# Performance work log

Hardware: AMD Instinct MI355X
Metric: run time of the kernel (lower is better)

Reference implementation:

```python
import jax, jax.numpy as jnp
import numpy as np

B, N, D, H, L, R = 2, 2048, 1024, 16, 3, 2
HID = int(D * 2.67)
NASH_ITERS, SINK_ITERS = 3, 10
EPS = 1e-6


def _rmsnorm(x, w):
    return x * w * jax.lax.rsqrt(jnp.mean(x * x, axis=-1, keepdims=True) + EPS)


def _sinkhorn(logits):
    # Sinkhorn-Knopp projection of exp(logits) to a doubly-stochastic matrix
    M = jnp.exp(logits)
    for _ in range(SINK_ITERS):
        M = M / jnp.sum(M, axis=1, keepdims=True)
        M = M / jnp.sum(M, axis=0, keepdims=True)
    return M


def _swiglu(x, wg, wu, wd):
    return (jax.nn.silu(x @ wg) * (x @ wu)) @ wd


def _attention(xl, wq, wk, Wv):
    # causal multi-head attention at one scale; V projection (Wv) is shared across scales
    b, n, d = xl.shape
    dh = d // H
    q = (xl @ wq).reshape(b, n, H, dh)
    k = (xl @ wk).reshape(b, n, H, dh)
    v = (xl @ Wv).reshape(b, n, H, dh)
    scores = jnp.einsum('bqhd,bkhd->bhqk', q, k) / jnp.asarray(float(np.sqrt(dh)), xl.dtype)
    mask = jnp.tril(jnp.ones((n, n), bool))
    scores = jnp.where(mask, scores, jnp.asarray(-1e9, xl.dtype))
    p = jax.nn.softmax(scores, axis=-1)
    return jnp.einsum('bhqk,bkhd->bqhd', p, v).reshape(b, n, d)


def _forward(x, norm_attn_w, norm_ffn_w, W_dec, Wq, Wk, Wv, Wo, agg_logits,
             w_gate, w_up, w_down, mhc_attn_logits, mhc_ffn_logits):
    residual = x
    xn = _rmsnorm(x, norm_attn_w)
    # 1) hierarchical decomposition: avg-pool by R each level, per-scale projection
    scales = []
    cur = xn
    for l in range(L):
        scales.append(cur @ W_dec[l])
        if l < L - 1:
            b, n, d = cur.shape
            cur = cur.reshape(b, n // R, R, d).mean(axis=2)
    # 2) multiscale causal attention with shared V; upsample back to N and project
    outs = []
    for l in range(L):
        o = _attention(scales[l], Wq[l], Wk[l], Wv)
        o = jnp.repeat(o, R ** l, axis=1)  # [B, N, D]
        outs.append(o @ Wo)
    Y = jnp.stack(outs, axis=0)  # [L, B, N, D]
    # 3) Nash aggregation: best-response iterations on scale weights
    w = jax.nn.softmax(agg_logits)
    for _ in range(NASH_ITERS):
        y_bar = jnp.einsum('l,lbnd->bnd', w, Y)
        u = -jnp.mean((Y - y_bar[None]) ** 2, axis=(1, 2, 3))  # [L] payoffs
        w = jax.nn.softmax(agg_logits + u)
    attn_out = jnp.einsum('l,lbnd->bnd', w, Y)
    aux_loss = jnp.sum(w * jnp.log(w * L + 1e-9))  # KL(w || uniform)
    # 4) mHC residual mixing (attention branch): doubly-stochastic convex mix
    P = _sinkhorn(mhc_attn_logits)
    x = P[0, 0] * residual + P[0, 1] * attn_out
    # 5) SwiGLU FFN + mHC residual (FFN branch)
    residual = x
    xn = _rmsnorm(x, norm_ffn_w)
    ffn_out = _swiglu(xn, w_gate, w_up, w_down)
    P2 = _sinkhorn(mhc_ffn_logits)
    x = P2[0, 0] * residual + P2[0, 1] * ffn_out
    return x, aux_loss


def setup_inputs() -> dict:
    key = jax.random.key(0)
    ks = jax.random.split(key, 16)
    init = 0.02
    s = lambda i, shape: jax.random.normal(ks[i], shape, jnp.float32) * init
    return {
        'x': jax.random.normal(ks[0], (B, N, D), jnp.float32),
        'norm_attn_w': jnp.ones((D,), jnp.float32),
        'norm_ffn_w': jnp.ones((D,), jnp.float32),
        'W_dec': s(1, (L, D, D)),
        'Wq': s(2, (L, D, D)),
        'Wk': s(3, (L, D, D)),
        'Wv': s(4, (D, D)),
        'Wo': s(5, (D, D)),
        'agg_logits': jnp.zeros((L,), jnp.float32),
        'w_gate': s(6, (D, HID)),
        'w_up': s(7, (D, HID)),
        'w_down': s(8, (HID, D)),
        'mhc_attn_logits': jnp.zeros((2, 2), jnp.float32),
        'mhc_ffn_logits': jnp.zeros((2, 2), jnp.float32),
    }


def reference(x, norm_attn_w, norm_ffn_w, W_dec, Wq, Wk, Wv, Wo, agg_logits,
              w_gate, w_up, w_down, mhc_attn_logits, mhc_ffn_logits):
    return _forward(x, norm_attn_w, norm_ffn_w, W_dec, Wq, Wk, Wv, Wo, agg_logits,
                    w_gate, w_up, w_down, mhc_attn_logits, mhc_ffn_logits)
```

## Files before the change

kernel.cpp:

```cpp
#include <hip/hip_runtime.h>
#include <stdint.h>


#define B_   2
#define N_   2048
#define D_   1024
#define H_   16
#define DH_  64
#define HID_ 2734
#define HIDP 2816
#define CNT  (B_*N_*D_)
#define LOG2E 1.4426950408889634f

typedef unsigned short u16;
typedef __attribute__((ext_vector_type(8))) short short8;
typedef __attribute__((ext_vector_type(4))) float f32x4;
typedef __attribute__((ext_vector_type(4))) uint16_t u16x4;

__device__ __forceinline__ u16 f2bf(float f) {
  uint32_t u = __builtin_bit_cast(uint32_t, f);
  u += 0x7fffu + ((u >> 16) & 1u);
  return (u16)(u >> 16);
}
__device__ __forceinline__ float bf2f(u16 h) {
  uint32_t u = ((uint32_t)h) << 16;
  return __builtin_bit_cast(float, u);
}
__device__ __forceinline__ uint32_t pkbf(float a, float b) {
  return (uint32_t)f2bf(a) | ((uint32_t)f2bf(b) << 16);
}
__device__ __forceinline__ void gload_lds16(const void* g, void* l) {
  __builtin_amdgcn_global_load_lds(
      (const __attribute__((address_space(1))) uint32_t*)g,
      (__attribute__((address_space(3))) uint32_t*)l, 16, 0, 0);
}

__global__ __launch_bounds__(256) void wprep_k(const float* __restrict__ Wdec, const float* __restrict__ Wq,
                                               const float* __restrict__ Wk, const float* __restrict__ Wv,
                                               const float* __restrict__ Wo, const float* __restrict__ Wg,
                                               const float* __restrict__ Wu, const float* __restrict__ Wdn,
                                               u16* __restrict__ A_wp, u16* __restrict__ WdecB,
                                               u16* __restrict__ WoT, u16* __restrict__ BTgu,
                                               u16* __restrict__ WdnT, float* __restrict__ SCb) {
  const int bid = blockIdx.x;
  if (bid >= 21760) {
    int bid0 = bid - 21760;
    int row = (bid0 < 2) ? (5454 + bid0) : (5470 + (bid0 - 2));
    u16x4 zz; zz[0]=0; zz[1]=0; zz[2]=0; zz[3]=0;
    *(u16x4*)(BTgu + (size_t)row*1024 + threadIdx.x*4) = zz;
    return;
  }
  if (bid >= 18688) {
    if (bid == 18688 && threadIdx.x < 64) SCb[threadIdx.x] = 0.f;
    int i = (bid - 18688)*1024 + threadIdx.x*4;
    float4 v = *(const float4*)(Wdec + i);
    u16x4 o; o[0]=f2bf(v.x); o[1]=f2bf(v.y); o[2]=f2bf(v.z); o[3]=f2bf(v.w);
    *(u16x4*)(WdecB + i) = o;
    return;
  }
  const float* src; u16* dst; int K, N, KP; float scale; int imode; int bx, by;
  if (bid < 9216) {
    int j = bid >> 10, t = bid & 1023; bx = t & 31; by = t >> 5;
    int l = j / 3, which = j - l*3;
    src = which==0 ? Wq + (size_t)l*1048576 : which==1 ? Wk + (size_t)l*1048576 : Wv;
    dst = A_wp + (size_t)(l*3072 + which*1024)*1024;
    K = 1024; N = 1024; KP = 1024; scale = (which==0) ? 0.125f*LOG2E : 1.f; imode = 0;
  } else if (bid < 10240) {
    int t = bid - 9216; bx = t & 31; by = t >> 5;
    src = Wo; dst = WoT; K=1024; N=1024; KP=1024; scale=1.f; imode=0;
  } else if (bid < 13056) {
    int t = bid - 10240; bx = t % 88; by = t / 88;
    src = Wg; dst = BTgu; K=1024; N=HID_; KP=1024; scale=1.f; imode=1;
  } else if (bid < 15872) {
    int t = bid - 13056; bx = t % 88; by = t / 88;
    src = Wu; dst = BTgu; K=1024; N=HID_; KP=1024; scale=1.f; imode=2;
  } else {
    int t = bid - 15872; bx = t & 31; by = t >> 5;
    src = Wdn; dst = WdnT; K=HID_; N=1024; KP=HIDP; scale=1.f; imode=0;
  }
  __shared__ float tt[32][33];
  const int tx = threadIdx.x & 31, ty = threadIdx.x >> 5;
  const int nb = bx*32, kb = by*32;
  #pragma unroll
  for (int i = 0; i < 4; i++) {
    int k = kb + ty + i*8, n = nb + tx;
    tt[ty + i*8][tx] = (k < K && n < N) ? src[(size_t)k * N + n] * scale : 0.f;
  }
  __syncthreads();
  #pragma unroll
  for (int i = 0; i < 4; i++) {
    int n = nb + ty + i*8, k = kb + tx;
    int r;
    if (imode == 0) r = n;
    else if (imode == 1) r = ((n>>4)<<5) + (n&15);
    else r = ((n>>4)<<5) + 16 + (n&15);
    dst[(size_t)r * KP + k] = f2bf(tt[tx][ty + i*8]);
  }
}

__global__ __launch_bounds__(256) void rmsA_k(const float* __restrict__ x, const float* __restrict__ w,
                                              u16* __restrict__ xn, u16* __restrict__ xp1) {
  const int j = blockIdx.x;
  const float* xr0 = x + (size_t)(2*j) * D_;
  const float* xr1 = xr0 + D_;
  float a0[4], a1[4], wv[4];
  float ss0 = 0.f, ss1 = 0.f;
  #pragma unroll
  for (int i = 0; i < 4; i++) {
    int c = threadIdx.x + i*256;
    a0[i] = xr0[c]; a1[i] = xr1[c]; wv[i] = w[c];
    ss0 += a0[i]*a0[i]; ss1 += a1[i]*a1[i];
  }
  #pragma unroll
  for (int o = 1; o < 64; o <<= 1) { ss0 += __shfl_xor(ss0, o); ss1 += __shfl_xor(ss1, o); }
  __shared__ float r0[4], r1[4];
  if ((threadIdx.x & 63) == 0) { r0[threadIdx.x >> 6] = ss0; r1[threadIdx.x >> 6] = ss1; }
  __syncthreads();
  float sc0 = rsqrtf((r0[0]+r0[1]+r0[2]+r0[3]) * (1.f/D_) + 1e-6f);
  float sc1 = rsqrtf((r1[0]+r1[1]+r1[2]+r1[3]) * (1.f/D_) + 1e-6f);
  #pragma unroll
  for (int i = 0; i < 4; i++) {
    int c = threadIdx.x + i*256;
    float xa = a0[i]*wv[i]*sc0, xb = a1[i]*wv[i]*sc1;
    xn[(size_t)(2*j)*D_ + c]     = f2bf(xa);
    xn[(size_t)(2*j)*D_ + D_ + c] = f2bf(xb);
    xp1[(size_t)j*D_ + c] = f2bf(0.5f*(xa + xb));
  }
}

__global__ __launch_bounds__(256) void pool_k(const u16* __restrict__ in, u16* __restrict__ out, int lg) {
  const int No = 1 << lg;
  const int total4 = B_ * No * 256;
  for (int i = blockIdx.x*256 + threadIdx.x; i < total4; i += gridDim.x*256) {
    int d4 = i & 255; int j = (i >> 8) & (No - 1); int b = i >> (8 + lg);
    size_t src = ((size_t)(b*2*No + 2*j) << 10) + d4*4;
    u16x4 a = *(const u16x4*)(in + src);
    u16x4 c = *(const u16x4*)(in + src + 1024);
    u16x4 o;
    #pragma unroll
    for (int t = 0; t < 4; t++) o[t] = f2bf(0.5f * (bf2f(a[t]) + bf2f(c[t])));
    *(u16x4*)(out + (size_t)i*4) = o;
  }
}

template<int MT, int MODE>
__global__ __launch_bounds__(256, 2) void gemm_t(const u16* __restrict__ A, const u16* __restrict__ BT,
                                                 void* __restrict__ Cv, void* __restrict__ Cv2,
                                                 const float* __restrict__ X1,
                                                 const float* __restrict__ SCp,
                                                 int N, int K, int t1, int t2, unsigned int bt_stride) {
  static_assert(MT == 4, "counted vmcnt(8) assumes MT+4 == 8 staging loads");
  __shared__ __align__(16) u16 As[2][MT*32*64];
  __shared__ __align__(16) u16 Bs[2][128*64];
  const int tid = threadIdx.x;
  const int lane = tid & 63, wid = tid >> 6;
  const int quad = lane >> 4, c16 = lane & 15;
  const int y = blockIdx.y;
  const int m0 = y * (MT*32), n0 = blockIdx.x * 128;
  const int wm = wid >> 1, wn = wid & 1;
  const int level = (y >= t2) ? 2 : ((y >= t1) ? 1 : 0);
  BT += (size_t)level * bt_stride;

  f32x4 acc[MT][4];
  #pragma unroll
  for (int i = 0; i < MT; i++)
    #pragma unroll
    for (int j = 0; j < 4; j++) acc[i][j] = f32x4{0.f,0.f,0.f,0.f};

  const int srow = lane >> 3;
  const int schunk = lane & 7;
  auto stage = [&](int k0, int p) {
    #pragma unroll
    for (int t = 0; t < MT; t++) {
      int idx = wid*MT + t;
      int row = idx*8 + srow;
      int g = (schunk ^ (row & 7)) * 8;
      gload_lds16(A + (size_t)(m0+row)*K + k0 + g, &As[p][idx*512]);
    }
    #pragma unroll
    for (int t = 0; t < 4; t++) {
      int idx = wid*4 + t;
      int row = idx*8 + srow;
      int g = (schunk ^ (row & 7)) * 8;
      gload_lds16(BT + (size_t)(n0+row)*K + k0 + g, &Bs[p][idx*512]);
    }
  };

  const int nk = K >> 6;
  stage(0, 0);
  for (int ki = 0; ki < nk; ki++) {
    const int p = ki & 1;
    if (ki + 1 < nk) {
      stage((ki + 1) << 6, p ^ 1);
      asm volatile("s_waitcnt vmcnt(8)" ::: "memory");
    } else {
      asm volatile("s_waitcnt vmcnt(0)" ::: "memory");
    }
    __builtin_amdgcn_s_barrier();
    __builtin_amdgcn_sched_barrier(0);
    __builtin_amdgcn_s_setprio(1);
    #pragma unroll
    for (int kh = 0; kh < 2; kh++) {
      short8 af[MT], bfr[4];
      #pragma unroll
      for (int mt = 0; mt < MT; mt++) {
        int ar = wm*(MT*16) + mt*16 + c16;
        int ck = (kh*4 + quad) ^ (ar & 7);
        af[mt] = *(const short8*)(&As[p][ar*64 + ck*8]);
      }
      #pragma unroll
      for (int nt = 0; nt < 4; nt++) {
        int br = wn*64 + nt*16 + c16;
        int ck = (kh*4 + quad) ^ (br & 7);
        bfr[nt] = *(const short8*)(&Bs[p][br*64 + ck*8]);
      }
      #pragma unroll
      for (int mt = 0; mt < MT; mt++)
        #pragma unroll
        for (int nt = 0; nt < 4; nt++)
          acc[mt][nt] = __builtin_amdgcn_mfma_f32_16x16x32_bf16(af[mt], bfr[nt], acc[mt][nt], 0, 0, 0);
    }
    __builtin_amdgcn_s_setprio(0);
    __builtin_amdgcn_sched_barrier(0);
    __builtin_amdgcn_s_barrier();
  }
  if (MODE == 1) {
    u16* C = (u16*)Cv;
    #pragma unroll
    for (int mt = 0; mt < MT; mt++)
      #pragma unroll
      for (int nt = 0; nt < 4; nt++)
        #pragma unroll
        for (int r = 0; r < 4; r++) {
          int row = m0 + wm*(MT*16) + mt*16 + quad*4 + r;
          int col = n0 + wn*64 + nt*16 + c16;
          C[(size_t)row * N + col] = f2bf(acc[mt][nt][r]);
        }
  } else if (MODE == 2) {
    float* C = (float*)Cv;
    const float q0 = SCp[11], q1 = SCp[12];
    #pragma unroll
    for (int mt = 0; mt < MT; mt++)
      #pragma unroll
      for (int nt = 0; nt < 4; nt++)
        #pragma unroll
        for (int r = 0; r < 4; r++) {
          int row = m0 + wm*(MT*16) + mt*16 + quad*4 + r;
          int col = n0 + wn*64 + nt*16 + c16;
          size_t o = (size_t)row * N + col;
          C[o] = q0 * X1[o] + q1 * acc[mt][nt][r];
        }
  } else if (MODE == 3) {
    u16* Hc = (u16*)Cv;
    const int hbase = (n0 >> 1) + wn*32;
    #pragma unroll
    for (int mt = 0; mt < MT; mt++)
      #pragma unroll
      for (int r = 0; r < 4; r++) {
        int row = m0 + wm*(MT*16) + mt*16 + quad*4 + r;
        #pragma unroll
        for (int pr = 0; pr < 2; pr++) {
          float g = acc[mt][2*pr][r], u = acc[mt][2*pr+1][r];
          float h = g / (1.f + __expf(-g)) * u;
          Hc[(size_t)row * HIDP + hbase + pr*16 + c16] = f2bf(h);
        }
      }
  } else {
    if (n0 < 2048) {
      u16* C = (u16*)Cv;
      #pragma unroll
      for (int mt = 0; mt < MT; mt++)
        #pragma unroll
        for (int nt = 0; nt < 4; nt++)
          #pragma unroll
          for (int r = 0; r < 4; r++) {
            int row = m0 + wm*(MT*16) + mt*16 + quad*4 + r;
            int col = n0 + wn*64 + nt*16 + c16;
            C[(size_t)row * N + col] = f2bf(acc[mt][nt][r]);
          }
    } else {
      const int Nl = 2048 >> level;
      const int lvbase = (level==0) ? 0 : (level==1) ? 4096 : 6144;
      const size_t vtoff = (level==0) ? 0 : (level==1) ? 4194304 : 6291456;
      u16* VT = (u16*)Cv2 + vtoff;
      #pragma unroll
      for (int mt = 0; mt < MT; mt++) {
        int rowg = m0 + wm*(MT*16) + mt*16 + quad*4;
        int nloc = rowg - lvbase;
        int b = nloc / Nl;
        int n = nloc - b*Nl;
        #pragma unroll
        for (int nt = 0; nt < 4; nt++) {
          int c = n0 - 2048 + wn*64 + nt*16 + c16;
          u16x4 o;
          o[0]=f2bf(acc[mt][nt][0]); o[1]=f2bf(acc[mt][nt][1]);
          o[2]=f2bf(acc[mt][nt][2]); o[3]=f2bf(acc[mt][nt][3]);
          *(u16x4*)(VT + ((size_t)(b*1024 + c))*Nl + n) = o;
        }
      }
    }
  }
}

__global__ __launch_bounds__(256) void flash_k(const u16* __restrict__ QKVg,
                                               const u16* __restrict__ VTg,
                                               u16* __restrict__ Og) {
  __shared__ __align__(16) u16 Kt[2][64*64];
  __shared__ __align__(16) u16 Vt[2][64*64];
  __shared__ __align__(16) u16 Ps[4][32*68];
  const int tid = threadIdx.x, lane = tid & 63, wid = tid >> 6;
  const int quad = lane >> 4, c16 = lane & 15;
  const int id = blockIdx.x;
  int qt, bh, Nl, rowbase; size_t vtoff;
  if (id < 512)      { qt = 15 - (id >> 5);            bh = id & 31;  Nl = 2048; rowbase = 0;    vtoff = 0; }
  else if (id < 768) { int t2 = id - 512; qt = 7 - (t2 >> 5); bh = t2 & 31; Nl = 1024; rowbase = 4096; vtoff = 4194304; }
  else               { int t2 = id - 768; qt = 3 - (t2 >> 5); bh = t2 & 31; Nl = 512;  rowbase = 6144; vtoff = 6291456; }
  const int b = bh >> 4, h = bh & 15;
  const u16* QK = QKVg + ((size_t)(rowbase + b*Nl)) * 3072 + h*64;
  u16* Ow = Og + ((size_t)(rowbase + b*Nl)) * 1024 + h*64;
  const u16* VT = VTg + vtoff + ((size_t)b*1024 + h*64) * (size_t)Nl;

  const int q0r = qt*128 + wid*32;
  short8 bq[2][2];
  #pragma unroll
  for (int qh = 0; qh < 2; qh++) {
    const u16* qp = QK + (size_t)(q0r + qh*16 + c16)*3072 + quad*8;
    bq[qh][0] = *(const short8*)qp;
    bq[qh][1] = *(const short8*)(qp + 32);
  }
  const int si0 = wid*2, si1 = si0 + 1;
  const int sr0 = si0*8 + (lane>>3), sr1 = si1*8 + (lane>>3);
  const int sg  = ((lane&7) ^ (lane>>3)) * 8;
  const u16* Ks0 = QK + 1024 + (size_t)sr0*3072 + sg;
  const u16* Ks1 = QK + 1024 + (size_t)sr1*3072 + sg;
  const u16* Vs0 = VT + (size_t)sr0*Nl + sg;
  const u16* Vs1 = VT + (size_t)sr1*Nl + sg;

  f32x4 oacc[2][4];
  f32x4 lacc[2];
  #pragma unroll
  for (int qh = 0; qh < 2; qh++) {
    lacc[qh] = f32x4{0.f,0.f,0.f,0.f};
    #pragma unroll
    for (int nt = 0; nt < 4; nt++) oacc[qh][nt] = f32x4{0.f,0.f,0.f,0.f};
  }

  auto stage = [&](int kt, int p) {
    const size_t ko = (size_t)kt * 64;
    gload_lds16(Ks0 + ko*3072, &Kt[p][si0*512]);
    gload_lds16(Ks1 + ko*3072, &Kt[p][si1*512]);
    gload_lds16(Vs0 + ko,      &Vt[p][si0*512]);
    gload_lds16(Vs1 + ko,      &Vt[p][si1*512]);
  };
  const int kmax_w = 2*qt + (wid >> 1);
  const int ktot   = 2*qt + 2;
  stage(0, 0);

  for (int kt = 0; kt < ktot; kt++) {
    const int p = kt & 1;
    __syncthreads();
    if (kt + 1 < ktot) stage(kt+1, p^1);
    if (kt > kmax_w) continue;

    f32x4 st[2][4];
    #pragma unroll
    for (int nt = 0; nt < 4; nt++) {
      int key = nt*16 + c16, x = key & 7;
      short8 a0 = *(const short8*)(&Kt[p][key*64 + ((quad    ) ^ x)*8]);
      short8 a1 = *(const short8*)(&Kt[p][key*64 + ((quad + 4) ^ x)*8]);
      #pragma unroll
      for (int qh = 0; qh < 2; qh++) {
        f32x4 s = f32x4{0.f,0.f,0.f,0.f};
        s = __builtin_amdgcn_mfma_f32_16x16x32_bf16(a0, bq[qh][0], s, 0, 0, 0);
        s = __builtin_amdgcn_mfma_f32_16x16x32_bf16(a1, bq[qh][1], s, 0, 0, 0);
        st[qh][nt] = s;
      }
    }
    if (kt >= 2*qt) {
      const int kb = kt*64;
      #pragma unroll
      for (int qh = 0; qh < 2; qh++) {
        const int qr = q0r + qh*16 + c16;
        #pragma unroll
        for (int nt = 0; nt < 4; nt++) {
          #pragma unroll
          for (int r = 0; r < 4; r++) {
            float e = __builtin_amdgcn_exp2f(st[qh][nt][r]);
            st[qh][nt][r] = (kb + nt*16 + quad*4 + r <= qr) ? e : 0.f;
          }
          lacc[qh] += st[qh][nt];
        }
      }
    } else {
      #pragma unroll
      for (int qh = 0; qh < 2; qh++)
        #pragma unroll
        for (int nt = 0; nt < 4; nt++) {
          #pragma unroll
          for (int r = 0; r < 4; r++) st[qh][nt][r] = __builtin_amdgcn_exp2f(st[qh][nt][r]);
          lacc[qh] += st[qh][nt];
        }
    }
    #pragma unroll
    for (int qh = 0; qh < 2; qh++) {
      const int prow = qh*16 + c16;
      #pragma unroll
      for (int nt = 0; nt < 4; nt++) {
        uint2 pk;
        pk.x = pkbf(st[qh][nt][0], st[qh][nt][1]);
        pk.y = pkbf(st[qh][nt][2], st[qh][nt][3]);
        *(uint2*)(&Ps[wid][prow*68 + nt*16 + quad*4]) = pk;
      }
    }
    short8 bp[2][2];
    #pragma unroll
    for (int qh = 0; qh < 2; qh++) {
      bp[qh][0] = *(const short8*)(&Ps[wid][(qh*16 + c16)*68 +      quad*8]);
      bp[qh][1] = *(const short8*)(&Ps[wid][(qh*16 + c16)*68 + 32 + quad*8]);
    }
    #pragma unroll
    for (int nt = 0; nt < 4; nt++) {
      int dh = nt*16 + c16, x = dh & 7;
      short8 a0 = *(const short8*)(&Vt[p][dh*64 + ((quad    ) ^ x)*8]);
      short8 a1 = *(const short8*)(&Vt[p][dh*64 + ((quad + 4) ^ x)*8]);
      #pragma unroll
      for (int qh = 0; qh < 2; qh++) {
        oacc[qh][nt] = __builtin_amdgcn_mfma_f32_16x16x32_bf16(a0, bp[qh][0], oacc[qh][nt], 0, 0, 0);
        oacc[qh][nt] = __builtin_amdgcn_mfma_f32_16x16x32_bf16(a1, bp[qh][1], oacc[qh][nt], 0, 0, 0);
      }
    }
  }
  #pragma unroll
  for (int qh = 0; qh < 2; qh++) {
    float ls = lacc[qh][0] + lacc[qh][1] + lacc[qh][2] + lacc[qh][3];
    ls += __shfl_xor(ls, 16);
    ls += __shfl_xor(ls, 32);
    const float rl = 1.f / ls;
    #pragma unroll
    for (int nt = 0; nt < 4; nt++) {
      uint2 o;
      o.x = pkbf(oacc[qh][nt][0]*rl, oacc[qh][nt][1]*rl);
      o.y = pkbf(oacc[qh][nt][2]*rl, oacc[qh][nt][3]*rl);
      *(uint2*)(Ow + (size_t)(q0r + qh*16 + c16)*1024 + nt*16 + quad*4) = o;
    }
  }
}

__global__ __launch_bounds__(256) void gram_k(const u16* __restrict__ Y0, const u16* __restrict__ Y1,
                                              const u16* __restrict__ Y2, float* __restrict__ G) {
  float a[6] = {0,0,0,0,0,0};
  const int total4 = CNT/4;
  for (int i = blockIdx.x*256 + threadIdx.x; i < total4; i += gridDim.x*256) {
    int d4 = i & 255; int n = (i >> 8) & (N_-1); int b = i >> 19;
    u16x4 y0v = *(const u16x4*)(Y0 + (size_t)i*4);
    u16x4 y1v = *(const u16x4*)(Y1 + (((size_t)(b*1024 + (n>>1))) << 10) + d4*4);
    u16x4 y2v = *(const u16x4*)(Y2 + (((size_t)(b*512  + (n>>2))) << 10) + d4*4);
    #pragma unroll
    for (int t = 0; t < 4; t++) {
      float y0 = bf2f(y0v[t]), y1 = bf2f(y1v[t]), y2 = bf2f(y2v[t]);
      a[0] += y0*y0; a[1] += y0*y1; a[2] += y0*y2;
      a[3] += y1*y1; a[4] += y1*y2; a[5] += y2*y2;
    }
  }
  __shared__ float red[4][6];
  const int lane = threadIdx.x & 63, wid = threadIdx.x >> 6;
  #pragma unroll
  for (int t = 0; t < 6; t++) {
    float v = a[t];
    v += __shfl_xor(v, 1);  v += __shfl_xor(v, 2);  v += __shfl_xor(v, 4);
    v += __shfl_xor(v, 8);  v += __shfl_xor(v, 16); v += __shfl_xor(v, 32);
    a[t] = v;
  }
  if (lane == 0)
    #pragma unroll
    for (int t = 0; t < 6; t++) red[wid][t] = a[t];
  __syncthreads();
  if (threadIdx.x < 6)
    atomicAdd(&G[threadIdx.x], red[0][threadIdx.x] + red[1][threadIdx.x] +
                               red[2][threadIdx.x] + red[3][threadIdx.x]);
}

__global__ void head_k(float* SC, const float* __restrict__ agg, const float* __restrict__ mA,
                       const float* __restrict__ mF, float* __restrict__ aux_out) {
  if (threadIdx.x != 0 || blockIdx.x != 0) return;
  float G[6];
  for (int t = 0; t < 6; t++) G[t] = SC[t];
  const int gi[3][3] = {{0,1,2},{1,3,4},{2,4,5}};
  float a[3] = {agg[0], agg[1], agg[2]};
  float w[3];
  {
    float m = fmaxf(a[0], fmaxf(a[1], a[2])); float s = 0.f;
    for (int l = 0; l < 3; l++) { w[l] = expf(a[l]-m); s += w[l]; }
    for (int l = 0; l < 3; l++) w[l] /= s;
  }
  const float inv = 1.f / (float)CNT;
  for (int it = 0; it < 3; it++) {
    float q = 0.f;
    for (int l = 0; l < 3; l++) for (int m2 = 0; m2 < 3; m2++) q += w[l]*w[m2]*G[gi[l][m2]];
    float z[3];
    for (int l = 0; l < 3; l++) {
      float dot = w[0]*G[gi[l][0]] + w[1]*G[gi[l][1]] + w[2]*G[gi[l][2]];
      z[l] = a[l] - (G[gi[l][l]] - 2.f*dot + q) * inv;
    }
    float m = fmaxf(z[0], fmaxf(z[1], z[2])); float s = 0.f;
    for (int l = 0; l < 3; l++) { w[l] = expf(z[l]-m); s += w[l]; }
    for (int l = 0; l < 3; l++) w[l] /= s;
  }
  SC[6] = w[0]; SC[7] = w[1]; SC[8] = w[2];
  aux_out[0] = w[0]*logf(w[0]*3.f + 1e-9f) + w[1]*logf(w[1]*3.f + 1e-9f) + w[2]*logf(w[2]*3.f + 1e-9f);
  for (int which = 0; which < 2; which++) {
    const float* Lg = which ? mF : mA;
    float M0 = expf(Lg[0]), M1 = expf(Lg[1]), M2 = expf(Lg[2]), M3 = expf(Lg[3]);
    for (int i2 = 0; i2 < 10; i2++) {
      float r0 = M0+M1, r1 = M2+M3; M0 /= r0; M1 /= r0; M2 /= r1; M3 /= r1;
      float c0 = M0+M2, c1 = M1+M3; M0 /= c0; M2 /= c0; M1 /= c1; M3 /= c1;
    }
    SC[9 + which*2] = M0; SC[10 + which*2] = M1;
  }
}

__global__ __launch_bounds__(256) void mixrms_k(const float* __restrict__ x, const u16* __restrict__ Y0,
                                                const u16* __restrict__ Y1, const u16* __restrict__ Y2,
                                                const float* __restrict__ SC, const float* __restrict__ w2,
                                                float* __restrict__ x1, u16* __restrict__ xn2) {
  const float w0 = SC[6], w1 = SC[7], ww2 = SC[8], p0 = SC[9], p1 = SC[10];
  const int i = blockIdx.x;
  const int b = i >> 11, n = i & 2047;
  const float* xr = x + (size_t)i * D_;
  const u16* y0 = Y0 + (size_t)i * D_;
  const u16* y1 = Y1 + (size_t)(b*1024 + (n>>1)) * D_;
  const u16* y2 = Y2 + (size_t)(b*512  + (n>>2)) * D_;
  float xv[4], wv[4];
  float ss = 0.f;
  #pragma unroll
  for (int t = 0; t < 4; t++) {
    int c = threadIdx.x + t*256;
    float v = p0*xr[c] + p1*(w0*bf2f(y0[c]) + w1*bf2f(y1[c]) + ww2*bf2f(y2[c]));
    xv[t] = v; wv[t] = w2[c]; ss += v*v;
    x1[(size_t)i*D_ + c] = v;
  }
  #pragma unroll
  for (int o = 1; o < 64; o <<= 1) ss += __shfl_xor(ss, o);
  __shared__ float red[4];
  if ((threadIdx.x & 63) == 0) red[threadIdx.x >> 6] = ss;
  __syncthreads();
  float sc = rsqrtf((red[0]+red[1]+red[2]+red[3]) * (1.f/D_) + 1e-6f);
  #pragma unroll
  for (int t = 0; t < 4; t++) {
    int c = threadIdx.x + t*256;
    xn2[(size_t)i*D_ + c] = f2bf(xv[t]*wv[t]*sc);
  }
}

extern "C" void kernel_launch(void* const* d_in, const int* in_sizes, int n_in,
                              void* d_out, int out_size, void* d_ws, size_t ws_size,
                              hipStream_t stream) {
  (void)in_sizes; (void)n_in; (void)out_size; (void)ws_size;
  const float* x    = (const float*)d_in[0];
  const float* nw1  = (const float*)d_in[1];
  const float* nw2  = (const float*)d_in[2];
  const float* Wdec = (const float*)d_in[3];
  const float* Wq   = (const float*)d_in[4];
  const float* Wk   = (const float*)d_in[5];
  const float* Wv   = (const float*)d_in[6];
  const float* Wo   = (const float*)d_in[7];
  const float* agg  = (const float*)d_in[8];
  const float* Wg   = (const float*)d_in[9];
  const float* Wu   = (const float*)d_in[10];
  const float* Wdn  = (const float*)d_in[11];
  const float* mA   = (const float*)d_in[12];
  const float* mF   = (const float*)d_in[13];
  float* out = (float*)d_out;

  char* ws = (char*)d_ws;
  size_t off = 0;
  auto take = [&](size_t b) { size_t r = off; off += (b + 255) & ~(size_t)255; return r; };

  u16* A_wp  = (u16*)(ws + take((size_t)9216*1024*2));
  u16* WdecB = (u16*)(ws + take((size_t)3*1024*1024*2));
  u16* Wqkv  = (u16*)(ws + take((size_t)9216*1024*2));
  u16* BTgu  = (u16*)(ws + take((size_t)5632*1024*2));
  u16* WdnT  = (u16*)(ws + take((size_t)HIDP*1024*2));
  u16* WoT   = (u16*)(ws + take((size_t)1024*1024*2));
  u16* xn_all = (u16*)(ws + take((size_t)7168*1024*2));
  float* x1  = (float*)(ws + take((size_t)CNT*4));
  float* SCb = (float*)(ws + take(256));
  char*  big = ws + take(88080384);
  u16*   QKV   = (u16*)big;
  u16*   VTa   = (u16*)(big + 44040192);
  u16*   Ob    = (u16*)(big + 58720256);
  u16*   YC    = (u16*)(big + 73400320);
  u16*   hbuf  = (u16*)big;

  dim3 blk(256);
  const int BIG = 1 << 30;

  wprep_k<<<21924, blk, 0, stream>>>(Wdec, Wq, Wk, Wv, Wo, Wg, Wu, Wdn,
                                     A_wp, WdecB, WoT, BTgu, WdnT, SCb);
  gemm_t<4,1><<<dim3(8, 72), blk, 0, stream>>>(A_wp, WdecB, Wqkv, nullptr, nullptr, nullptr,
                                               1024, 1024, 24, 48, 1024u*1024u);
  rmsA_k<<<2048, blk, 0, stream>>>(x, nw1, xn_all, xn_all + (size_t)4096*1024);
  pool_k<<<512, blk, 0, stream>>>(xn_all + (size_t)4096*1024, xn_all + (size_t)6144*1024, 9);
  gemm_t<4,4><<<dim3(24, 56), blk, 0, stream>>>(xn_all, Wqkv, QKV, VTa, nullptr, nullptr,
                                                3072, 1024, 32, 48, 3072u*1024u);
  flash_k<<<896, blk, 0, stream>>>(QKV, VTa, Ob);
  gemm_t<4,1><<<dim3(8, 56), blk, 0, stream>>>(Ob, WoT, YC, nullptr, nullptr, nullptr,
                                               1024, 1024, BIG, BIG, 0u);
  u16* YC1 = YC + (size_t)4096*1024;
  u16* YC2 = YC + (size_t)6144*1024;
  gram_k<<<1024, blk, 0, stream>>>(YC, YC1, YC2, SCb);
  head_k<<<1, 64, 0, stream>>>(SCb, agg, mA, mF, out + CNT);
  mixrms_k<<<4096, blk, 0, stream>>>(x, YC, YC1, YC2, SCb, nw2, x1, xn_all);
  gemm_t<4,3><<<dim3(44, 32), blk, 0, stream>>>(xn_all, BTgu, hbuf, nullptr, nullptr, nullptr,
                                                5632, 1024, BIG, BIG, 0u);
  gemm_t<4,2><<<dim3(8, 32), blk, 0, stream>>>(hbuf, WdnT, out, nullptr, x1, SCb,
                                               1024, HIDP, BIG, BIG, 0u);
}
```

Before: 494.1 us.

## Fuse weight prep, Wqkv GEMM, RMSNorm and pooling into one launch; merge gram/head

Splits weight preparation so only the Q/K/V/Wdec conversion runs first. A single heterogeneous kernel then runs the Wdec-folded QKV weight GEMM alongside the Wo/FFN weight transposes and a fused RMSNorm that also emits both pooled levels directly. The gram reduction and head computation are merged using a last-block atomic counter, and the down-projection GEMM switches to MT=2 tiles with twice as many row blocks. The goal is fewer launches and better overlap of independent small work, at the cost of a larger mixed-shape kernel and a grid-completion counter that relies on the SCb zeroing done earlier in the first kernel.

```diff
diff --git a/kernel.cpp b/kernel.cpp
--- a/kernel.cpp
+++ b/kernel.cpp
@@ -35,111 +35,205 @@
       (__attribute__((address_space(3))) uint32_t*)l, 16, 0, 0);
 }
 
-__global__ __launch_bounds__(256) void wprep_k(const float* __restrict__ Wdec, const float* __restrict__ Wq,
-                                               const float* __restrict__ Wk, const float* __restrict__ Wv,
-                                               const float* __restrict__ Wo, const float* __restrict__ Wg,
-                                               const float* __restrict__ Wu, const float* __restrict__ Wdn,
-                                               u16* __restrict__ A_wp, u16* __restrict__ WdecB,
-                                               u16* __restrict__ WoT, u16* __restrict__ BTgu,
-                                               u16* __restrict__ WdnT, float* __restrict__ SCb) {
+__global__ __launch_bounds__(256) void wprep1_k(const float* __restrict__ Wdec, const float* __restrict__ Wq,
+                                                const float* __restrict__ Wk, const float* __restrict__ Wv,
+                                                u16* __restrict__ A_wp, u16* __restrict__ WdecB,
+                                                float* __restrict__ SCb) {
   const int bid = blockIdx.x;
-  if (bid >= 21760) {
-    int bid0 = bid - 21760;
-    int row = (bid0 < 2) ? (5454 + bid0) : (5470 + (bid0 - 2));
-    u16x4 zz; zz[0]=0; zz[1]=0; zz[2]=0; zz[3]=0;
-    *(u16x4*)(BTgu + (size_t)row*1024 + threadIdx.x*4) = zz;
-    return;
-  }
-  if (bid >= 18688) {
-    if (bid == 18688 && threadIdx.x < 64) SCb[threadIdx.x] = 0.f;
-    int i = (bid - 18688)*1024 + threadIdx.x*4;
+  if (bid >= 9216) {
+    if (bid == 9216 && threadIdx.x < 64) SCb[threadIdx.x] = 0.f;
+    int i = (bid - 9216)*1024 + threadIdx.x*4;
     float4 v = *(const float4*)(Wdec + i);
     u16x4 o; o[0]=f2bf(v.x); o[1]=f2bf(v.y); o[2]=f2bf(v.z); o[3]=f2bf(v.w);
     *(u16x4*)(WdecB + i) = o;
     return;
   }
-  const float* src; u16* dst; int K, N, KP; float scale; int imode; int bx, by;
-  if (bid < 9216) {
-    int j = bid >> 10, t = bid & 1023; bx = t & 31; by = t >> 5;
-    int l = j / 3, which = j - l*3;
-    src = which==0 ? Wq + (size_t)l*1048576 : which==1 ? Wk + (size_t)l*1048576 : Wv;
-    dst = A_wp + (size_t)(l*3072 + which*1024)*1024;
-    K = 1024; N = 1024; KP = 1024; scale = (which==0) ? 0.125f*LOG2E : 1.f; imode = 0;
-  } else if (bid < 10240) {
-    int t = bid - 9216; bx = t & 31; by = t >> 5;
-    src = Wo; dst = WoT; K=1024; N=1024; KP=1024; scale=1.f; imode=0;
-  } else if (bid < 13056) {
-    int t = bid - 10240; bx = t % 88; by = t / 88;
-    src = Wg; dst = BTgu; K=1024; N=HID_; KP=1024; scale=1.f; imode=1;
-  } else if (bid < 15872) {
-    int t = bid - 13056; bx = t % 88; by = t / 88;
-    src = Wu; dst = BTgu; K=1024; N=HID_; KP=1024; scale=1.f; imode=2;
-  } else {
-    int t = bid - 15872; bx = t & 31; by = t >> 5;
-    src = Wdn; dst = WdnT; K=HID_; N=1024; KP=HIDP; scale=1.f; imode=0;
-  }
+  int j = bid >> 10, t = bid & 1023;
+  int bx = t & 31, by = t >> 5;
+  int l = j / 3, which = j - l*3;
+  const float* src = which==0 ? Wq + (size_t)l*1048576 : which==1 ? Wk + (size_t)l*1048576 : Wv;
+  u16* dst = A_wp + (size_t)(l*3072 + which*1024)*1024;
+  const float scale = (which==0) ? 0.125f*LOG2E : 1.f;
   __shared__ float tt[32][33];
   const int tx = threadIdx.x & 31, ty = threadIdx.x >> 5;
   const int nb = bx*32, kb = by*32;
   #pragma unroll
-  for (int i = 0; i < 4; i++) {
-    int k = kb + ty + i*8, n = nb + tx;
-    tt[ty + i*8][tx] = (k < K && n < N) ? src[(size_t)k * N + n] * scale : 0.f;
-  }
+  for (int i = 0; i < 4; i++)
+    tt[ty + i*8][tx] = src[(size_t)(kb + ty + i*8) * 1024 + nb + tx] * scale;
   __syncthreads();
   #pragma unroll
-  for (int i = 0; i < 4; i++) {
-    int n = nb + ty + i*8, k = kb + tx;
-    int r;
-    if (imode == 0) r = n;
-    else if (imode == 1) r = ((n>>4)<<5) + (n&15);
-    else r = ((n>>4)<<5) + 16 + (n&15);
-    dst[(size_t)r * KP + k] = f2bf(tt[tx][ty + i*8]);
-  }
-}
-
-__global__ __launch_bounds__(256) void rmsA_k(const float* __restrict__ x, const float* __restrict__ w,
-                                              u16* __restrict__ xn, u16* __restrict__ xp1) {
-  const int j = blockIdx.x;
-  const float* xr0 = x + (size_t)(2*j) * D_;
-  const float* xr1 = xr0 + D_;
-  float a0[4], a1[4], wv[4];
-  float ss0 = 0.f, ss1 = 0.f;
-  #pragma unroll
-  for (int i = 0; i < 4; i++) {
-    int c = threadIdx.x + i*256;
-    a0[i] = xr0[c]; a1[i] = xr1[c]; wv[i] = w[c];
-    ss0 += a0[i]*a0[i]; ss1 += a1[i]*a1[i];
-  }
-  #pragma unroll
-  for (int o = 1; o < 64; o <<= 1) { ss0 += __shfl_xor(ss0, o); ss1 += __shfl_xor(ss1, o); }
-  __shared__ float r0[4], r1[4];
-  if ((threadIdx.x & 63) == 0) { r0[threadIdx.x >> 6] = ss0; r1[threadIdx.x >> 6] = ss1; }
-  __syncthreads();
-  float sc0 = rsqrtf((r0[0]+r0[1]+r0[2]+r0[3]) * (1.f/D_) + 1e-6f);
-  float sc1 = rsqrtf((r1[0]+r1[1]+r1[2]+r1[3]) * (1.f/D_) + 1e-6f);
-  #pragma unroll
-  for (int i = 0; i < 4; i++) {
-    int c = threadIdx.x + i*256;
-    float xa = a0[i]*wv[i]*sc0, xb = a1[i]*wv[i]*sc1;
-    xn[(size_t)(2*j)*D_ + c]     = f2bf(xa);
-    xn[(size_t)(2*j)*D_ + D_ + c] = f2bf(xb);
-    xp1[(size_t)j*D_ + c] = f2bf(0.5f*(xa + xb));
-  }
-}
-
-__global__ __launch_bounds__(256) void pool_k(const u16* __restrict__ in, u16* __restrict__ out, int lg) {
-  const int No = 1 << lg;
-  const int total4 = B_ * No * 256;
-  for (int i = blockIdx.x*256 + threadIdx.x; i < total4; i += gridDim.x*256) {
-    int d4 = i & 255; int j = (i >> 8) & (No - 1); int b = i >> (8 + lg);
-    size_t src = ((size_t)(b*2*No + 2*j) << 10) + d4*4;
-    u16x4 a = *(const u16x4*)(in + src);
-    u16x4 c = *(const u16x4*)(in + src + 1024);
-    u16x4 o;
-    #pragma unroll
-    for (int t = 0; t < 4; t++) o[t] = f2bf(0.5f * (bf2f(a[t]) + bf2f(c[t])));
-    *(u16x4*)(out + (size_t)i*4) = o;
+  for (int i = 0; i < 4; i++)
+    dst[(size_t)(nb + ty + i*8) * 1024 + kb + tx] = f2bf(tt[tx][ty + i*8]);
+}
+
+__global__ __launch_bounds__(256, 2) void mega_k(const u16* __restrict__ A_wp, const u16* __restrict__ WdecB,
+                                                 u16* __restrict__ Wqkv,
+                                                 const float* __restrict__ Wo, const float* __restrict__ Wg,
+                                                 const float* __restrict__ Wu, const float* __restrict__ Wdn,
+                                                 u16* __restrict__ WoT, u16* __restrict__ BTgu,
+                                                 u16* __restrict__ WdnT,
+                                                 const float* __restrict__ x, const float* __restrict__ nw1,
+                                                 u16* __restrict__ xn, u16* __restrict__ xp1,
+                                                 u16* __restrict__ xp2) {
+  const int bid = blockIdx.x;
+  const int tid = threadIdx.x;
+  if (bid < 576) {
+    __shared__ __align__(16) u16 As[2][128*64];
+    __shared__ __align__(16) u16 Bs[2][128*64];
+    const int lane = tid & 63, wid = tid >> 6;
+    const int quad = lane >> 4, c16 = lane & 15;
+    const int bx = bid & 7, by = bid >> 3;
+    const int m0 = by * 128, n0 = bx * 128;
+    const int wm = wid >> 1, wn = wid & 1;
+    const int level = (by >= 48) ? 2 : ((by >= 24) ? 1 : 0);
+    const u16* BT = WdecB + (size_t)level * 1048576;
+    const u16* A = A_wp;
+
+    f32x4 acc[4][4];
+    #pragma unroll
+    for (int i = 0; i < 4; i++)
+      #pragma unroll
+      for (int j = 0; j < 4; j++) acc[i][j] = f32x4{0.f,0.f,0.f,0.f};
+
+    const int srow = lane >> 3, schunk = lane & 7;
+    auto stage = [&](int k0, int p) {
+      #pragma unroll
+      for (int t = 0; t < 4; t++) {
+        int idx = wid*4 + t;
+        int row = idx*8 + srow;
+        int g = (schunk ^ (row & 7)) * 8;
+        gload_lds16(A + (size_t)(m0+row)*1024 + k0 + g, &As[p][idx*512]);
+      }
+      #pragma unroll
+      for (int t = 0; t < 4; t++) {
+        int idx = wid*4 + t;
+        int row = idx*8 + srow;
+        int g = (schunk ^ (row & 7)) * 8;
+        gload_lds16(BT + (size_t)(n0+row)*1024 + k0 + g, &Bs[p][idx*512]);
+      }
+    };
+    stage(0, 0);
+    for (int ki = 0; ki < 16; ki++) {
+      const int p = ki & 1;
+      if (ki + 1 < 16) {
+        stage((ki + 1) << 6, p ^ 1);
+        asm volatile("s_waitcnt vmcnt(8)" ::: "memory");
+      } else {
+        asm volatile("s_waitcnt vmcnt(0)" ::: "memory");
+      }
+      __builtin_amdgcn_s_barrier();
+      __builtin_amdgcn_sched_barrier(0);
+      __builtin_amdgcn_s_setprio(1);
+      #pragma unroll
+      for (int kh = 0; kh < 2; kh++) {
+        short8 af[4], bfr[4];
+        #pragma unroll
+        for (int mt = 0; mt < 4; mt++) {
+          int ar = wm*64 + mt*16 + c16;
+          int ck = (kh*4 + quad) ^ (ar & 7);
+          af[mt] = *(const short8*)(&As[p][ar*64 + ck*8]);
+        }
+        #pragma unroll
+        for (int nt = 0; nt < 4; nt++) {
+          int br = wn*64 + nt*16 + c16;
+          int ck = (kh*4 + quad) ^ (br & 7);
+          bfr[nt] = *(const short8*)(&Bs[p][br*64 + ck*8]);
+        }
+        #pragma unroll
+        for (int mt = 0; mt < 4; mt++)
+          #pragma unroll
+          for (int nt = 0; nt < 4; nt++)
+            acc[mt][nt] = __builtin_amdgcn_mfma_f32_16x16x32_bf16(af[mt], bfr[nt], acc[mt][nt], 0, 0, 0);
+      }
+      __builtin_amdgcn_s_setprio(0);
+      __builtin_amdgcn_sched_barrier(0);
+      __builtin_amdgcn_s_barrier();
+    }
+    #pragma unroll
+    for (int mt = 0; mt < 4; mt++)
+      #pragma unroll
+      for (int nt = 0; nt < 4; nt++)
+        #pragma unroll
+        for (int r = 0; r < 4; r++) {
+          int row = m0 + wm*64 + mt*16 + quad*4 + r;
+          int col = n0 + wn*64 + nt*16 + c16;
+          Wqkv[(size_t)row * 1024 + col] = f2bf(acc[mt][nt][r]);
+        }
+    return;
+  }
+  const int t2v = bid - 576;
+  if (t2v < 9472) {
+    const float* src; u16* dst; int K, N, KP, imode, bx, by;
+    if (t2v < 1024)      { src = Wo;  dst = WoT;  K=1024; N=1024; KP=1024; imode=0; bx=t2v&31; by=t2v>>5; }
+    else if (t2v < 3840) { int t = t2v-1024; src = Wg; dst = BTgu; K=1024; N=HID_; KP=1024; imode=1; bx=t%88; by=t/88; }
+    else if (t2v < 6656) { int t = t2v-3840; src = Wu; dst = BTgu; K=1024; N=HID_; KP=1024; imode=2; bx=t%88; by=t/88; }
+    else                 { int t = t2v-6656; src = Wdn; dst = WdnT; K=HID_; N=1024; KP=HIDP; imode=0; bx=t&31; by=t>>5; }
+    __shared__ float tt[32][33];
+    const int tx = tid & 31, ty = tid >> 5;
+    const int nb = bx*32, kb = by*32;
+    #pragma unroll
+    for (int i = 0; i < 4; i++) {
+      int k = kb + ty + i*8, n = nb + tx;
+      tt[ty + i*8][tx] = (k < K && n < N) ? src[(size_t)k * N + n] : 0.f;
+    }
+    __syncthreads();
+    #pragma unroll
+    for (int i = 0; i < 4; i++) {
+      int n = nb + ty + i*8, k = kb + tx;
+      int r;
+      if (imode == 0) r = n;
+      else if (imode == 1) r = ((n>>4)<<5) + (n&15);
+      else r = ((n>>4)<<5) + 16 + (n&15);
+      dst[(size_t)r * KP + k] = f2bf(tt[tx][ty + i*8]);
+    }
+    return;
+  }
+  if (t2v < 9636) {
+    int b0 = t2v - 9472;
+    int row = (b0 < 2) ? (5454 + b0) : (5470 + (b0 - 2));
+    u16x4 zz; zz[0]=0; zz[1]=0; zz[2]=0; zz[3]=0;
+    *(u16x4*)(BTgu + (size_t)row*1024 + tid*4) = zz;
+    return;
+  }
+  {
+    const int j = t2v - 9636;
+    const float* xr = x + (size_t)(4*j) * D_;
+    float a0[4], a1[4], a2[4], a3[4], wv[4];
+    float s0=0.f, s1=0.f, s2=0.f, s3=0.f;
+    #pragma unroll
+    for (int i = 0; i < 4; i++) {
+      int c = tid + i*256;
+      wv[i] = nw1[c];
+      a0[i] = xr[c]; a1[i] = xr[D_+c]; a2[i] = xr[2*D_+c]; a3[i] = xr[3*D_+c];
+      s0 += a0[i]*a0[i]; s1 += a1[i]*a1[i]; s2 += a2[i]*a2[i]; s3 += a3[i]*a3[i];
+    }
+    #pragma unroll
+    for (int o = 1; o < 64; o <<= 1) {
+      s0 += __shfl_xor(s0, o); s1 += __shfl_xor(s1, o);
+      s2 += __shfl_xor(s2, o); s3 += __shfl_xor(s3, o);
+    }
+    __shared__ float rr[4][4];
+    if ((tid & 63) == 0) { int w = tid >> 6; rr[w][0]=s0; rr[w][1]=s1; rr[w][2]=s2; rr[w][3]=s3; }
+    __syncthreads();
+    float m0v = rr[0][0]+rr[1][0]+rr[2][0]+rr[3][0];
+    float m1v = rr[0][1]+rr[1][1]+rr[2][1]+rr[3][1];
+    float m2v = rr[0][2]+rr[1][2]+rr[2][2]+rr[3][2];
+    float m3v = rr[0][3]+rr[1][3]+rr[2][3]+rr[3][3];
+    float c0 = rsqrtf(m0v*(1.f/D_) + 1e-6f), c1 = rsqrtf(m1v*(1.f/D_) + 1e-6f);
+    float c2 = rsqrtf(m2v*(1.f/D_) + 1e-6f), c3 = rsqrtf(m3v*(1.f/D_) + 1e-6f);
+    #pragma unroll
+    for (int i = 0; i < 4; i++) {
+      int c = tid + i*256;
+      float v0 = a0[i]*wv[i]*c0, v1 = a1[i]*wv[i]*c1;
+      float v2 = a2[i]*wv[i]*c2, v3 = a3[i]*wv[i]*c3;
+      xn[(size_t)(4*j)*D_ + c]          = f2bf(v0);
+      xn[(size_t)(4*j)*D_ + D_ + c]     = f2bf(v1);
+      xn[(size_t)(4*j)*D_ + 2*D_ + c]   = f2bf(v2);
+      xn[(size_t)(4*j)*D_ + 3*D_ + c]   = f2bf(v3);
+      xp1[(size_t)(2*j)*D_ + c]         = f2bf(0.5f*(v0 + v1));
+      xp1[(size_t)(2*j)*D_ + D_ + c]    = f2bf(0.5f*(v2 + v3));
+      xp2[(size_t)j*D_ + c]             = f2bf(0.25f*(v0 + v1 + v2 + v3));
+    }
   }
 }
 
@@ -149,7 +243,7 @@
                                                  const float* __restrict__ X1,
                                                  const float* __restrict__ SCp,
                                                  int N, int K, int t1, int t2, unsigned int bt_stride) {
-  static_assert(MT == 4, "counted vmcnt(8) assumes MT+4 == 8 staging loads");
+  static_assert(MT == 4 || MT == 2, "vmcnt count assumes MT+4 staging loads");
   __shared__ __align__(16) u16 As[2][MT*32*64];
   __shared__ __align__(16) u16 Bs[2][128*64];
   const int tid = threadIdx.x;
@@ -192,7 +286,8 @@
     const int p = ki & 1;
     if (ki + 1 < nk) {
       stage((ki + 1) << 6, p ^ 1);
-      asm volatile("s_waitcnt vmcnt(8)" ::: "memory");
+      if constexpr (MT == 4) asm volatile("s_waitcnt vmcnt(8)" ::: "memory");
+      else                   asm volatile("s_waitcnt vmcnt(6)" ::: "memory");
     } else {
       asm volatile("s_waitcnt vmcnt(0)" ::: "memory");
     }
@@ -446,8 +541,11 @@
   }
 }
 
-__global__ __launch_bounds__(256) void gram_k(const u16* __restrict__ Y0, const u16* __restrict__ Y1,
-                                              const u16* __restrict__ Y2, float* __restrict__ G) {
+__global__ __launch_bounds__(256) void gramhead_k(const u16* __restrict__ Y0, const u16* __restrict__ Y1,
+                                                  const u16* __restrict__ Y2, float* __restrict__ G,
+                                                  int* __restrict__ done,
+                                                  const float* __restrict__ agg, const float* __restrict__ mA,
+                                                  const float* __restrict__ mF, float* __restrict__ aux_out) {
   float a[6] = {0,0,0,0,0,0};
   const int total4 = CNT/4;
   for (int i = blockIdx.x*256 + threadIdx.x; i < total4; i += gridDim.x*256) {
@@ -478,44 +576,47 @@
   if (threadIdx.x < 6)
     atomicAdd(&G[threadIdx.x], red[0][threadIdx.x] + red[1][threadIdx.x] +
                                red[2][threadIdx.x] + red[3][threadIdx.x]);
-}
-
-__global__ void head_k(float* SC, const float* __restrict__ agg, const float* __restrict__ mA,
-                       const float* __restrict__ mF, float* __restrict__ aux_out) {
-  if (threadIdx.x != 0 || blockIdx.x != 0) return;
-  float G[6];
-  for (int t = 0; t < 6; t++) G[t] = SC[t];
-  const int gi[3][3] = {{0,1,2},{1,3,4},{2,4,5}};
-  float a[3] = {agg[0], agg[1], agg[2]};
-  float w[3];
-  {
-    float m = fmaxf(a[0], fmaxf(a[1], a[2])); float s = 0.f;
-    for (int l = 0; l < 3; l++) { w[l] = expf(a[l]-m); s += w[l]; }
-    for (int l = 0; l < 3; l++) w[l] /= s;
-  }
-  const float inv = 1.f / (float)CNT;
-  for (int it = 0; it < 3; it++) {
-    float q = 0.f;
-    for (int l = 0; l < 3; l++) for (int m2 = 0; m2 < 3; m2++) q += w[l]*w[m2]*G[gi[l][m2]];
-    float z[3];
-    for (int l = 0; l < 3; l++) {
-      float dot = w[0]*G[gi[l][0]] + w[1]*G[gi[l][1]] + w[2]*G[gi[l][2]];
-      z[l] = a[l] - (G[gi[l][l]] - 2.f*dot + q) * inv;
-    }
-    float m = fmaxf(z[0], fmaxf(z[1], z[2])); float s = 0.f;
-    for (int l = 0; l < 3; l++) { w[l] = expf(z[l]-m); s += w[l]; }
-    for (int l = 0; l < 3; l++) w[l] /= s;
-  }
-  SC[6] = w[0]; SC[7] = w[1]; SC[8] = w[2];
-  aux_out[0] = w[0]*logf(w[0]*3.f + 1e-9f) + w[1]*logf(w[1]*3.f + 1e-9f) + w[2]*logf(w[2]*3.f + 1e-9f);
-  for (int which = 0; which < 2; which++) {
-    const float* Lg = which ? mF : mA;
-    float M0 = expf(Lg[0]), M1 = expf(Lg[1]), M2 = expf(Lg[2]), M3 = expf(Lg[3]);
-    for (int i2 = 0; i2 < 10; i2++) {
-      float r0 = M0+M1, r1 = M2+M3; M0 /= r0; M1 /= r0; M2 /= r1; M3 /= r1;
-      float c0 = M0+M2, c1 = M1+M3; M0 /= c0; M2 /= c0; M1 /= c1; M3 /= c1;
-    }
-    SC[9 + which*2] = M0; SC[10 + which*2] = M1;
+  __threadfence();
+  __shared__ int lastf;
+  if (threadIdx.x == 0) lastf = (atomicAdd(done, 1) == (int)gridDim.x - 1);
+  __syncthreads();
+  if (lastf && threadIdx.x == 0) {
+    float Gv[6];
+    for (int t = 0; t < 6; t++)
+      Gv[t] = __hip_atomic_load(&G[t], __ATOMIC_RELAXED, __HIP_MEMORY_SCOPE_AGENT);
+    float* SC = G;
+    const int gi[3][3] = {{0,1,2},{1,3,4},{2,4,5}};
+    float av[3] = {agg[0], agg[1], agg[2]};
+    float w[3];
+    {
+      float m = fmaxf(av[0], fmaxf(av[1], av[2])); float s = 0.f;
+      for (int l = 0; l < 3; l++) { w[l] = expf(av[l]-m); s += w[l]; }
+      for (int l = 0; l < 3; l++) w[l] /= s;
+    }
+    const float inv = 1.f / (float)CNT;
+    for (int it = 0; it < 3; it++) {
+      float q = 0.f;
+      for (int l = 0; l < 3; l++) for (int m2 = 0; m2 < 3; m2++) q += w[l]*w[m2]*Gv[gi[l][m2]];
+      float z[3];
+      for (int l = 0; l < 3; l++) {
+        float dot = w[0]*Gv[gi[l][0]] + w[1]*Gv[gi[l][1]] + w[2]*Gv[gi[l][2]];
+        z[l] = av[l] - (Gv[gi[l][l]] - 2.f*dot + q) * inv;
+      }
+      float m = fmaxf(z[0], fmaxf(z[1], z[2])); float s = 0.f;
+      for (int l = 0; l < 3; l++) { w[l] = expf(z[l]-m); s += w[l]; }
+      for (int l = 0; l < 3; l++) w[l] /= s;
+    }
+    SC[6] = w[0]; SC[7] = w[1]; SC[8] = w[2];
+    aux_out[0] = w[0]*logf(w[0]*3.f + 1e-9f) + w[1]*logf(w[1]*3.f + 1e-9f) + w[2]*logf(w[2]*3.f + 1e-9f);
+    for (int which = 0; which < 2; which++) {
+      const float* Lg = which ? mF : mA;
+      float M0 = expf(Lg[0]), M1 = expf(Lg[1]), M2 = expf(Lg[2]), M3 = expf(Lg[3]);
+      for (int i2 = 0; i2 < 10; i2++) {
+        float r0 = M0+M1, r1 = M2+M3; M0 /= r0; M1 /= r0; M2 /= r1; M3 /= r1;
+        float c0 = M0+M2, c1 = M1+M3; M0 /= c0; M2 /= c0; M1 /= c1; M3 /= c1;
+      }
+      SC[9 + which*2] = M0; SC[10 + which*2] = M1;
+    }
   }
 }
 
@@ -592,15 +693,16 @@
   u16*   YC    = (u16*)(big + 73400320);
   u16*   hbuf  = (u16*)big;
 
+  u16* xp1 = xn_all + (size_t)4096*1024;
+  u16* xp2 = xn_all + (size_t)6144*1024;
+  int* done = (int*)SCb + 15;
+
   dim3 blk(256);
   const int BIG = 1 << 30;
 
-  wprep_k<<<21924, blk, 0, stream>>>(Wdec, Wq, Wk, Wv, Wo, Wg, Wu, Wdn,
-                                     A_wp, WdecB, WoT, BTgu, WdnT, SCb);
-  gemm_t<4,1><<<dim3(8, 72), blk, 0, stream>>>(A_wp, WdecB, Wqkv, nullptr, nullptr, nullptr,
-                                               1024, 1024, 24, 48, 1024u*1024u);
-  rmsA_k<<<2048, blk, 0, stream>>>(x, nw1, xn_all, xn_all + (size_t)4096*1024);
-  pool_k<<<512, blk, 0, stream>>>(xn_all + (size_t)4096*1024, xn_all + (size_t)6144*1024, 9);
+  wprep1_k<<<12288, blk, 0, stream>>>(Wdec, Wq, Wk, Wv, A_wp, WdecB, SCb);
+  mega_k<<<11236, blk, 0, stream>>>(A_wp, WdecB, Wqkv, Wo, Wg, Wu, Wdn,
+                                    WoT, BTgu, WdnT, x, nw1, xn_all, xp1, xp2);
   gemm_t<4,4><<<dim3(24, 56), blk, 0, stream>>>(xn_all, Wqkv, QKV, VTa, nullptr, nullptr,
                                                 3072, 1024, 32, 48, 3072u*1024u);
   flash_k<<<896, blk, 0, stream>>>(QKV, VTa, Ob);
@@ -608,11 +710,10 @@
                                                1024, 1024, BIG, BIG, 0u);
   u16* YC1 = YC + (size_t)4096*1024;
   u16* YC2 = YC + (size_t)6144*1024;
-  gram_k<<<1024, blk, 0, stream>>>(YC, YC1, YC2, SCb);
-  head_k<<<1, 64, 0, stream>>>(SCb, agg, mA, mF, out + CNT);
+  gramhead_k<<<1024, blk, 0, stream>>>(YC, YC1, YC2, SCb, done, agg, mA, mF, out + CNT);
   mixrms_k<<<4096, blk, 0, stream>>>(x, YC, YC1, YC2, SCb, nw2, x1, xn_all);
   gemm_t<4,3><<<dim3(44, 32), blk, 0, stream>>>(xn_all, BTgu, hbuf, nullptr, nullptr, nullptr,
                                                 5632, 1024, BIG, BIG, 0u);
-  gemm_t<4,2><<<dim3(8, 32), blk, 0, stream>>>(hbuf, WdnT, out, nullptr, x1, SCb,
+  gemm_t<2,2><<<dim3(8, 64), blk, 0, stream>>>(hbuf, WdnT, out, nullptr, x1, SCb,
                                                1024, HIDP, BIG, BIG, 0u);
 }
```

Result: slower. 536.0 us (+8.5%).
